# Kernel optimization log

Measured on AMD Instinct MI355X. Metric: run time of the kernel, lower is better.

## Reference

```python
import jax, jax.numpy as jnp
import numpy as np

T = 10            # inference steps (PCLayer.T)
LOCAL_LR = 0.001  # local_learning_rate
CLAMP = 1.0       # PCLayer.clamp_value


def setup_inputs() -> dict:
    key = jax.random.key(0)
    k1, k2 = jax.random.split(key)
    B, S, H_out, H_in = 8, 1024, 3072, 768
    target_activity = jax.random.normal(k1, (B, S, H_out), dtype=jnp.float32)
    # nn.Linear(H_in, H_out) weight: [H_out, H_in]
    W = jax.random.normal(k2, (H_out, H_in), dtype=jnp.float32) * (1.0 / np.sqrt(H_in))
    b = jnp.zeros((H_out,), dtype=jnp.float32)
    return {"target_activity": target_activity, "W": W, "b": b}


def reference(target_activity, W, b):
    # PCLayer forward, layer_type='fc1' (linear): T-step energy-gradient
    # fixed-point inference on latent x of shape [B, S, H_in].
    B, S, _ = target_activity.shape
    H_in = W.shape[1]
    x0 = jnp.zeros((B, S, H_in), dtype=target_activity.dtype)  # x_init

    def step(x, _):
        mu = jnp.einsum('bsi,oi->bso', x, W) + b       # prediction [B,S,H_out]
        err = target_activity - mu                      # prediction error
        # x <- x - lr * dE/dx, E = 0.5*||err||^2  =>  dE/dx = -err @ W
        x = x + LOCAL_LR * jnp.einsum('bso,oi->bsi', err, W)
        x = jnp.clip(x, -CLAMP, CLAMP)
        return x, None

    x, _ = jax.lax.scan(step, x0, None, length=T)
    return x
```

## Files before the change

kernel.cpp:

```cpp
#include <hip/hip_runtime.h>
#include <stdint.h>


typedef short bf16x8 __attribute__((ext_vector_type(8)));
typedef float f32x4  __attribute__((ext_vector_type(4)));
typedef unsigned short u16;
typedef unsigned int uint_as1 __attribute__((address_space(1)));
typedef unsigned int uint_as3 __attribute__((address_space(3)));

__device__ __forceinline__ float bf2f(u16 u) {
  union { unsigned int i; float f; } x; x.i = ((unsigned int)u) << 16; return x.f;
}
__device__ __forceinline__ u16 f2bf(float f) {
  union { float f; unsigned int i; } x; x.f = f;
  unsigned int r = x.i + 0x7fffu + ((x.i >> 16) & 1u);
  return (u16)(r >> 16);
}
__device__ __forceinline__ void gl2lds16(const void* g, void* l) {
  __builtin_amdgcn_global_load_lds((uint_as1*)(uintptr_t)g,
                                   (uint_as3*)(uintptr_t)l, 16, 0, 0);
}

template<int NK, int EPI>
__global__ __launch_bounds__(256, 2)
void gemm_lds(const u16* __restrict__ A, const u16* __restrict__ B,
              float* __restrict__ Cf, u16* __restrict__ Cb,
              const u16* __restrict__ Yb, const float* __restrict__ biasp,
              float* __restrict__ cvec, float alpha, float beta, int K, int ldc)
{
  __shared__ u16 As[64 * 32 * NK];
  __shared__ u16 Bs[128 * 32 * NK];
  const int tid = threadIdx.x, w = tid >> 6, lane = tid & 63;
  const int lm = lane & 15, quad = lane >> 4;
  const int wm = w & 1, wn = w >> 1;
  const int m0 = blockIdx.x * 64, n0 = blockIdx.y * 128;
  const int r = lane >> 2, q = lane & 3;
  const u16* Ag = A + (long)(m0 + w * 16 + r) * K + q * 8;
  const u16* Bg = B + (long)(n0 + w * 32 + r) * K + q * 8;
  u16* Asl = As + w * 16 * 32;
  u16* Bsl = Bs + w * 1024;

  f32x4 acc[2][4] = {};

  for (int kk = 0; kk < K; kk += 32 * NK) {
#pragma unroll
    for (int h = 0; h < NK; ++h) {
      gl2lds16(Ag + kk + h * 32, Asl + h * 2048);
      gl2lds16(Bg + kk + h * 32, Bsl + h * 4096);
      gl2lds16(Bg + 16 * (long)K + kk + h * 32, Bsl + h * 4096 + 512);
    }
    __syncthreads();
#pragma unroll
    for (int h = 0; h < NK; ++h) {
      bf16x8 af[2], bv[4];
#pragma unroll
      for (int i = 0; i < 2; ++i)
        af[i] = *(const bf16x8*)(As + h * 2048 +
                                 (wm * 32 + i * 16 + lm) * 32 + quad * 8);
#pragma unroll
      for (int j = 0; j < 4; ++j)
        bv[j] = *(const bf16x8*)(Bs + h * 4096 +
                                 (wn * 64 + j * 16 + lm) * 32 + quad * 8);
#pragma unroll
      for (int i = 0; i < 2; ++i)
#pragma unroll
        for (int j = 0; j < 4; ++j)
          acc[i][j] = __builtin_amdgcn_mfma_f32_16x16x32_bf16(af[i], bv[j],
                                                              acc[i][j], 0, 0, 0);
    }
    __syncthreads();
  }

  const int rbase = m0 + wm * 32 + quad * 4;
  const int cbase = n0 + wn * 64 + lm;
  float bvals[4] = {};
  bool haveb = false;
  if constexpr (EPI == 3) {
#pragma unroll
    for (int j = 0; j < 4; ++j) bvals[j] = biasp[cbase + j * 16];
    haveb = (bvals[0] != 0.f) | (bvals[1] != 0.f) |
            (bvals[2] != 0.f) | (bvals[3] != 0.f);
  }
  float rowsum[2][4] = {};
#pragma unroll
  for (int i = 0; i < 2; ++i)
#pragma unroll
    for (int j = 0; j < 4; ++j) {
      const int col = cbase + j * 16;
#pragma unroll
      for (int rr = 0; rr < 4; ++rr) {
        const long idx = (long)(rbase + i * 16 + rr) * ldc + col;
        const float v = alpha * acc[i][j][rr];
        if constexpr (EPI == 3) {
          const u16 qv = f2bf(v + beta * bf2f(Yb[idx]));
          Cb[idx] = qv;
          rowsum[i][rr] += bf2f(qv) * bvals[j];
        } else if constexpr (EPI == 4) {
          Cb[idx] = f2bf(v + beta * Cf[idx]);
        } else {
          Cf[idx] = v;
          Cb[idx] = f2bf(v);
        }
      }
    }
  if constexpr (EPI == 3) {
    if (__any(haveb)) {
#pragma unroll
      for (int i = 0; i < 2; ++i)
#pragma unroll
        for (int rr = 0; rr < 4; ++rr) {
          float s = rowsum[i][rr];
          s += __shfl_xor(s, 1); s += __shfl_xor(s, 2);
          s += __shfl_xor(s, 4); s += __shfl_xor(s, 8);
          if (lm == 0) atomicAdd(&cvec[rbase + i * 16 + rr], s);
        }
    }
  }
}

__global__ void conv_w(const float* __restrict__ W, u16* __restrict__ WTb,
                       u16* __restrict__ Wb, float* __restrict__ cvec)
{
  __shared__ u16 lds[64 * 72];
  const int bt = blockIdx.x, tid = threadIdx.x;
  if (bt == 0) { cvec[tid] = 0.f; cvec[tid + 256] = 0.f; cvec[tid + 512] = 0.f; }
  const int o0 = (bt / 12) * 64, i0 = (bt % 12) * 64;
  const int ol = tid >> 2, cg4 = tid & 3;
#pragma unroll
  for (int p = 0; p < 4; ++p) {
    const float4 v = *(const float4*)(W + (long)(o0 + ol) * 768 + i0 + (cg4 + p * 4) * 4);
    const int ib = (cg4 + p * 4) * 4;
    lds[(ib + 0) * 72 + ol] = f2bf(v.x);
    lds[(ib + 1) * 72 + ol] = f2bf(v.y);
    lds[(ib + 2) * 72 + ol] = f2bf(v.z);
    lds[(ib + 3) * 72 + ol] = f2bf(v.w);
    ushort4 wo;
    wo.x = f2bf(v.x); wo.y = f2bf(v.y); wo.z = f2bf(v.z); wo.w = f2bf(v.w);
    ((ushort4*)(Wb + (long)(o0 + ol) * 768 + i0))[cg4 + p * 4] = wo;
  }
  __syncthreads();
  const int cl = tid >> 2, og = tid & 3;
  const u16* src = lds + cl * 72 + og * 16;
  u16* dst = WTb + (long)(i0 + cl) * 3072 + o0 + og * 16;
  ((ushort4*)dst)[0] = ((const ushort4*)src)[0];
  ((ushort4*)dst)[1] = ((const ushort4*)src)[1];
  ((ushort4*)dst)[2] = ((const ushort4*)src)[2];
  ((ushort4*)dst)[3] = ((const ushort4*)src)[3];
}

__global__ __launch_bounds__(256, 2)
void gemm_big(const float* __restrict__ T, const u16* __restrict__ B,
              const float* __restrict__ cvec, float* __restrict__ out)
{
  __shared__ u16 As[2 * 64 * 32];
  __shared__ u16 Bs[2 * 256 * 32];
  const int tid = threadIdx.x, w = tid >> 6, lane = tid & 63;
  const int lm = lane & 15, quad = lane >> 4;
  const int m0 = blockIdx.x * 64, n0 = blockIdx.y * 256;
  const int r = lane >> 2, q = lane & 3;
  const int qs = q ^ ((r >> 2) & 3);
  const u16* Bg = B + (long)(n0 + w * 64 + r) * 3072 + qs * 8;
  u16* Bsl = Bs + w * 64 * 32;
  const int arow = tid >> 4, kq = tid & 15;
  const float* Ag = T + (long)(m0 + arow) * 3072 + kq * 4;
  const int h_a = kq >> 3;
  const int chunk_a = ((kq & 7) >> 1) ^ ((arow >> 2) & 3);
  const int ks_a = chunk_a * 8 + (kq & 1) * 4;
  const int swr = (lm >> 2) & 3;

  f32x4 acc[4][4] = {};

  for (int kk = 0; kk < 3072; kk += 64) {
#pragma unroll
    for (int h = 0; h < 2; ++h)
#pragma unroll
      for (int l = 0; l < 4; ++l)
        gl2lds16(Bg + (long)(l * 16) * 3072 + kk + h * 32,
                 Bsl + h * 8192 + l * 512);
#pragma unroll
    for (int p = 0; p < 4; ++p) {
      const float4 v = *(const float4*)(Ag + (long)(p * 16) * 3072 + kk);
      short4 o;
      o.x = (short)f2bf(v.x); o.y = (short)f2bf(v.y);
      o.z = (short)f2bf(v.z); o.w = (short)f2bf(v.w);
      *(short4*)(As + h_a * 2048 + (arow + p * 16) * 32 + ks_a) = o;
    }
    __syncthreads();
#pragma unroll
    for (int h = 0; h < 2; ++h) {
      bf16x8 af[4], bv[4];
#pragma unroll
      for (int i = 0; i < 4; ++i)
        af[i] = *(const bf16x8*)(As + h * 2048 + (i * 16 + lm) * 32 +
                                 ((quad ^ swr) * 8));
#pragma unroll
      for (int j = 0; j < 4; ++j)
        bv[j] = *(const bf16x8*)(Bs + h * 8192 + (w * 64 + j * 16 + lm) * 32 +
                                 ((quad ^ swr) * 8));
#pragma unroll
      for (int i = 0; i < 4; ++i)
#pragma unroll
        for (int j = 0; j < 4; ++j)
          acc[i][j] = __builtin_amdgcn_mfma_f32_16x16x32_bf16(af[i], bv[j],
                                                              acc[i][j], 0, 0, 0);
    }
    __syncthreads();
  }

  const int rbase = m0 + quad * 4;
  const int cbase = n0 + w * 64 + lm;
  float cj[4];
#pragma unroll
  for (int j = 0; j < 4; ++j) cj[j] = cvec[cbase + j * 16];
#pragma unroll
  for (int i = 0; i < 4; ++i)
#pragma unroll
    for (int j = 0; j < 4; ++j)
#pragma unroll
      for (int rr = 0; rr < 4; ++rr)
        out[(long)(rbase + i * 16 + rr) * 768 + cbase + j * 16] =
            acc[i][j][rr] - cj[j];
}

extern "C" void kernel_launch(void* const* d_in, const int* in_sizes, int n_in,
                              void* d_out, int out_size, void* d_ws, size_t ws_size,
                              hipStream_t stream)
{
  const float* t    = (const float*)d_in[0];
  const float* W    = (const float*)d_in[1];
  const float* bias = (const float*)d_in[2];
  float* out = (float*)d_out;

  char* p = (char*)d_ws;
  u16*   WTb  = (u16*)(p + 0);
  u16*   Wb   = (u16*)(p + 4718592);
  float* Ef   = (float*)(p + 9437184);
  u16*   Eb   = (u16*)(p + 11796480);
  u16*   Spb  = (u16*)(p + 12976128);
  u16*   WMTb = (u16*)(p + 14155776);
  float* cvec = (float*)(p + 18874368);

  const float lr = 0.001f;

  conv_w<<<576, 256, 0, stream>>>(W, WTb, Wb, cvec);
  gemm_lds<2, 5><<<dim3(12, 6), 256, 0, stream>>>(
      WTb, WTb, Ef, Eb, nullptr, nullptr, nullptr, lr, 0.f, 3072, 768);
  gemm_lds<2, 4><<<dim3(12, 6), 256, 0, stream>>>(
      Eb, Eb, Ef, Spb, nullptr, nullptr, nullptr, 120.f, -45.f, 768, 768);
  gemm_lds<2, 3><<<dim3(12, 24), 256, 0, stream>>>(
      Spb, Wb, nullptr, WMTb, WTb, bias, cvec, lr, 0.01f, 768, 3072);
  gemm_big<<<dim3(128, 3), 256, 0, stream>>>(t, WMTb, cvec, out);
}
```

Measured before the change: 290.5 us.

## Double-buffer B tiles and prefetch A in gemm_big, raise NK in gemm_lds

gemm_big now keeps two LDS buffers for the B tile. It issues the next tile's global-to-LDS loads and the next A float4 loads before the current MFMA work, so memory latency overlaps with compute and one barrier per iteration can be dropped. The XOR swizzle on LDS reads and writes is removed, which simplifies addressing but may bring back LDS bank conflicts. The gemm_lds launches also change the NK template parameter from 2 to 4. Doubling the B buffer raises LDS use, which could lower occupancy.

```diff
diff --git a/kernel.cpp b/kernel.cpp
--- a/kernel.cpp
+++ b/kernel.cpp
@@ -153,50 +153,62 @@
               const float* __restrict__ cvec, float* __restrict__ out)
 {
   __shared__ u16 As[2 * 64 * 32];
-  __shared__ u16 Bs[2 * 256 * 32];
+  __shared__ u16 Bs[2][2 * 256 * 32];
   const int tid = threadIdx.x, w = tid >> 6, lane = tid & 63;
   const int lm = lane & 15, quad = lane >> 4;
   const int m0 = blockIdx.x * 64, n0 = blockIdx.y * 256;
   const int r = lane >> 2, q = lane & 3;
-  const int qs = q ^ ((r >> 2) & 3);
-  const u16* Bg = B + (long)(n0 + w * 64 + r) * 3072 + qs * 8;
-  u16* Bsl = Bs + w * 64 * 32;
+  const u16* Bg = B + (long)(n0 + w * 64 + r) * 3072 + q * 8;
   const int arow = tid >> 4, kq = tid & 15;
   const float* Ag = T + (long)(m0 + arow) * 3072 + kq * 4;
-  const int h_a = kq >> 3;
-  const int chunk_a = ((kq & 7) >> 1) ^ ((arow >> 2) & 3);
-  const int ks_a = chunk_a * 8 + (kq & 1) * 4;
-  const int swr = (lm >> 2) & 3;
+  const int h_a = kq >> 3, ks_a = (kq & 7) * 4;
+  u16* As_dst = As + h_a * 2048 + arow * 32 + ks_a;
 
   f32x4 acc[4][4] = {};
-
+  float4 av[4];
+
+#pragma unroll
+  for (int p = 0; p < 4; ++p)
+    av[p] = *(const float4*)(Ag + (long)(p * 16) * 3072);
+#pragma unroll
+  for (int h = 0; h < 2; ++h)
+#pragma unroll
+    for (int l = 0; l < 4; ++l)
+      gl2lds16(Bg + (long)(l * 16) * 3072 + h * 32,
+               Bs[0] + h * 8192 + w * 2048 + l * 512);
+#pragma unroll
+  for (int p = 0; p < 4; ++p) {
+    short4 o;
+    o.x = (short)f2bf(av[p].x); o.y = (short)f2bf(av[p].y);
+    o.z = (short)f2bf(av[p].z); o.w = (short)f2bf(av[p].w);
+    *(short4*)(As_dst + p * 512) = o;
+  }
+
+  int buf = 0;
   for (int kk = 0; kk < 3072; kk += 64) {
-#pragma unroll
-    for (int h = 0; h < 2; ++h)
-#pragma unroll
-      for (int l = 0; l < 4; ++l)
-        gl2lds16(Bg + (long)(l * 16) * 3072 + kk + h * 32,
-                 Bsl + h * 8192 + l * 512);
-#pragma unroll
-    for (int p = 0; p < 4; ++p) {
-      const float4 v = *(const float4*)(Ag + (long)(p * 16) * 3072 + kk);
-      short4 o;
-      o.x = (short)f2bf(v.x); o.y = (short)f2bf(v.y);
-      o.z = (short)f2bf(v.z); o.w = (short)f2bf(v.w);
-      *(short4*)(As + h_a * 2048 + (arow + p * 16) * 32 + ks_a) = o;
-    }
     __syncthreads();
+    const bool haveNext = (kk + 64 < 3072);
+    if (haveNext) {
+#pragma unroll
+      for (int h = 0; h < 2; ++h)
+#pragma unroll
+        for (int l = 0; l < 4; ++l)
+          gl2lds16(Bg + (long)(l * 16) * 3072 + kk + 64 + h * 32,
+                   Bs[buf ^ 1] + h * 8192 + w * 2048 + l * 512);
+#pragma unroll
+      for (int p = 0; p < 4; ++p)
+        av[p] = *(const float4*)(Ag + (long)(p * 16) * 3072 + kk + 64);
+    }
+    const u16* Bsb = Bs[buf];
 #pragma unroll
     for (int h = 0; h < 2; ++h) {
       bf16x8 af[4], bv[4];
 #pragma unroll
       for (int i = 0; i < 4; ++i)
-        af[i] = *(const bf16x8*)(As + h * 2048 + (i * 16 + lm) * 32 +
-                                 ((quad ^ swr) * 8));
+        af[i] = *(const bf16x8*)(As + h * 2048 + (i * 16 + lm) * 32 + quad * 8);
 #pragma unroll
       for (int j = 0; j < 4; ++j)
-        bv[j] = *(const bf16x8*)(Bs + h * 8192 + (w * 64 + j * 16 + lm) * 32 +
-                                 ((quad ^ swr) * 8));
+        bv[j] = *(const bf16x8*)(Bsb + h * 8192 + (w * 64 + j * 16 + lm) * 32 + quad * 8);
 #pragma unroll
       for (int i = 0; i < 4; ++i)
 #pragma unroll
@@ -204,7 +216,17 @@
           acc[i][j] = __builtin_amdgcn_mfma_f32_16x16x32_bf16(af[i], bv[j],
                                                               acc[i][j], 0, 0, 0);
     }
-    __syncthreads();
+    if (haveNext) {
+      __syncthreads();
+#pragma unroll
+      for (int p = 0; p < 4; ++p) {
+        short4 o;
+        o.x = (short)f2bf(av[p].x); o.y = (short)f2bf(av[p].y);
+        o.z = (short)f2bf(av[p].z); o.w = (short)f2bf(av[p].w);
+        *(short4*)(As_dst + p * 512) = o;
+      }
+      buf ^= 1;
+    }
   }
 
   const int rbase = m0 + quad * 4;
@@ -243,11 +265,11 @@
   const float lr = 0.001f;
 
   conv_w<<<576, 256, 0, stream>>>(W, WTb, Wb, cvec);
-  gemm_lds<2, 5><<<dim3(12, 6), 256, 0, stream>>>(
+  gemm_lds<4, 5><<<dim3(12, 6), 256, 0, stream>>>(
       WTb, WTb, Ef, Eb, nullptr, nullptr, nullptr, lr, 0.f, 3072, 768);
-  gemm_lds<2, 4><<<dim3(12, 6), 256, 0, stream>>>(
+  gemm_lds<4, 4><<<dim3(12, 6), 256, 0, stream>>>(
       Eb, Eb, Ef, Spb, nullptr, nullptr, nullptr, 120.f, -45.f, 768, 768);
-  gemm_lds<2, 3><<<dim3(12, 24), 256, 0, stream>>>(
+  gemm_lds<4, 3><<<dim3(12, 24), 256, 0, stream>>>(
       Spb, Wb, nullptr, WMTb, WTb, bias, cvec, lr, 0.01f, 768, 3072);
   gemm_big<<<dim3(128, 3), 256, 0, stream>>>(t, WMTb, cvec, out);
 }
```

Result: faster. 281.4 us (-3.1%).

## Overlap target bf16 conversion with small GEMMs and reuse gemm_lds for final GEMM

Applied to the files above, without the earlier changes.

The fp32→bf16 conversion of the large target tensor, with bias subtracted, is split into slices run by extra blocks appended to the conv_w and three small GEMM launches. Those launches use only 72–288 blocks and leave most CUs idle, so the conversion uses that spare capacity. The final GEMM drops the specialized gemm_big, which converted fp32 inline, and becomes a gemm_lds instance with a new epilogue reading the pre-converted bf16 buffer. It also raises NK to 4 for all GEMMs. The cost is an extra 50MB bf16 buffer in workspace that is written and then read back.

```diff
diff --git a/kernel.cpp b/kernel.cpp
--- a/kernel.cpp
+++ b/kernel.cpp
@@ -21,19 +21,42 @@
                                    (uint_as3*)(uintptr_t)l, 16, 0, 0);
 }
 
+__device__ __forceinline__ void conv_slice(const float* __restrict__ t,
+                                           const float* __restrict__ bias,
+                                           u16* __restrict__ tb,
+                                           int blockUnit, int tid)
+{
+  const long i4 = (long)blockUnit * 256 + tid;
+  const float4 v = ((const float4*)t)[i4];
+  const float4 bb = ((const float4*)bias)[(int)(i4 % 768)];
+  ushort4 o;
+  o.x = f2bf(v.x - bb.x); o.y = f2bf(v.y - bb.y);
+  o.z = f2bf(v.z - bb.z); o.w = f2bf(v.w - bb.w);
+  ((ushort4*)tb)[i4] = o;
+}
+
 template<int NK, int EPI>
 __global__ __launch_bounds__(256, 2)
 void gemm_lds(const u16* __restrict__ A, const u16* __restrict__ B,
               float* __restrict__ Cf, u16* __restrict__ Cb,
               const u16* __restrict__ Yb, const float* __restrict__ biasp,
-              float* __restrict__ cvec, float alpha, float beta, int K, int ldc)
+              float* __restrict__ cvec, float alpha, float beta,
+              int K, int ldc, int nbx, int gemmBlocks, int convBase,
+              const float* __restrict__ tsrc, const float* __restrict__ tbias,
+              u16* __restrict__ tbdst)
 {
   __shared__ u16 As[64 * 32 * NK];
   __shared__ u16 Bs[128 * 32 * NK];
-  const int tid = threadIdx.x, w = tid >> 6, lane = tid & 63;
+  const int tid = threadIdx.x;
+  if ((int)blockIdx.x >= gemmBlocks) {
+    conv_slice(tsrc, tbias, tbdst, (int)blockIdx.x - gemmBlocks + convBase, tid);
+    return;
+  }
+  const int bx = (int)blockIdx.x % nbx, by = (int)blockIdx.x / nbx;
+  const int w = tid >> 6, lane = tid & 63;
   const int lm = lane & 15, quad = lane >> 4;
   const int wm = w & 1, wn = w >> 1;
-  const int m0 = blockIdx.x * 64, n0 = blockIdx.y * 128;
+  const int m0 = bx * 64, n0 = by * 128;
   const int r = lane >> 2, q = lane & 3;
   const u16* Ag = A + (long)(m0 + w * 16 + r) * K + q * 8;
   const u16* Bg = B + (long)(n0 + w * 32 + r) * K + q * 8;
@@ -80,6 +103,11 @@
     for (int j = 0; j < 4; ++j) bvals[j] = biasp[cbase + j * 16];
     haveb = (bvals[0] != 0.f) | (bvals[1] != 0.f) |
             (bvals[2] != 0.f) | (bvals[3] != 0.f);
+  }
+  float cj[4];
+  if constexpr (EPI == 6) {
+#pragma unroll
+    for (int j = 0; j < 4; ++j) cj[j] = cvec[cbase + j * 16];
   }
   float rowsum[2][4] = {};
 #pragma unroll
@@ -97,9 +125,11 @@
           rowsum[i][rr] += bf2f(qv) * bvals[j];
         } else if constexpr (EPI == 4) {
           Cb[idx] = f2bf(v + beta * Cf[idx]);
-        } else {
+        } else if constexpr (EPI == 5) {
           Cf[idx] = v;
           Cb[idx] = f2bf(v);
+        } else {
+          Cf[idx] = v - cj[j];
         }
       }
     }
@@ -118,11 +148,14 @@
   }
 }
 
-__global__ void conv_w(const float* __restrict__ W, u16* __restrict__ WTb,
-                       u16* __restrict__ Wb, float* __restrict__ cvec)
+__global__ void conv_w(const float* __restrict__ W, const float* __restrict__ t,
+                       const float* __restrict__ bias, u16* __restrict__ WTb,
+                       u16* __restrict__ Wb, u16* __restrict__ tb,
+                       float* __restrict__ cvec)
 {
   __shared__ u16 lds[64 * 72];
   const int bt = blockIdx.x, tid = threadIdx.x;
+  if (bt >= 576) { conv_slice(t, bias, tb, bt - 576, tid); return; }
   if (bt == 0) { cvec[tid] = 0.f; cvec[tid + 256] = 0.f; cvec[tid + 512] = 0.f; }
   const int o0 = (bt / 12) * 64, i0 = (bt % 12) * 64;
   const int ol = tid >> 2, cg4 = tid & 3;
@@ -148,80 +181,6 @@
   ((ushort4*)dst)[3] = ((const ushort4*)src)[3];
 }
 
-__global__ __launch_bounds__(256, 2)
-void gemm_big(const float* __restrict__ T, const u16* __restrict__ B,
-              const float* __restrict__ cvec, float* __restrict__ out)
-{
-  __shared__ u16 As[2 * 64 * 32];
-  __shared__ u16 Bs[2 * 256 * 32];
-  const int tid = threadIdx.x, w = tid >> 6, lane = tid & 63;
-  const int lm = lane & 15, quad = lane >> 4;
-  const int m0 = blockIdx.x * 64, n0 = blockIdx.y * 256;
-  const int r = lane >> 2, q = lane & 3;
-  const int qs = q ^ ((r >> 2) & 3);
-  const u16* Bg = B + (long)(n0 + w * 64 + r) * 3072 + qs * 8;
-  u16* Bsl = Bs + w * 64 * 32;
-  const int arow = tid >> 4, kq = tid & 15;
-  const float* Ag = T + (long)(m0 + arow) * 3072 + kq * 4;
-  const int h_a = kq >> 3;
-  const int chunk_a = ((kq & 7) >> 1) ^ ((arow >> 2) & 3);
-  const int ks_a = chunk_a * 8 + (kq & 1) * 4;
-  const int swr = (lm >> 2) & 3;
-
-  f32x4 acc[4][4] = {};
-
-  for (int kk = 0; kk < 3072; kk += 64) {
-#pragma unroll
-    for (int h = 0; h < 2; ++h)
-#pragma unroll
-      for (int l = 0; l < 4; ++l)
-        gl2lds16(Bg + (long)(l * 16) * 3072 + kk + h * 32,
-                 Bsl + h * 8192 + l * 512);
-#pragma unroll
-    for (int p = 0; p < 4; ++p) {
-      const float4 v = *(const float4*)(Ag + (long)(p * 16) * 3072 + kk);
-      short4 o;
-      o.x = (short)f2bf(v.x); o.y = (short)f2bf(v.y);
-      o.z = (short)f2bf(v.z); o.w = (short)f2bf(v.w);
-      *(short4*)(As + h_a * 2048 + (arow + p * 16) * 32 + ks_a) = o;
-    }
-    __syncthreads();
-#pragma unroll
-    for (int h = 0; h < 2; ++h) {
-      bf16x8 af[4], bv[4];
-#pragma unroll
-      for (int i = 0; i < 4; ++i)
-        af[i] = *(const bf16x8*)(As + h * 2048 + (i * 16 + lm) * 32 +
-                                 ((quad ^ swr) * 8));
-#pragma unroll
-      for (int j = 0; j < 4; ++j)
-        bv[j] = *(const bf16x8*)(Bs + h * 8192 + (w * 64 + j * 16 + lm) * 32 +
-                                 ((quad ^ swr) * 8));
-#pragma unroll
-      for (int i = 0; i < 4; ++i)
-#pragma unroll
-        for (int j = 0; j < 4; ++j)
-          acc[i][j] = __builtin_amdgcn_mfma_f32_16x16x32_bf16(af[i], bv[j],
-                                                              acc[i][j], 0, 0, 0);
-    }
-    __syncthreads();
-  }
-
-  const int rbase = m0 + quad * 4;
-  const int cbase = n0 + w * 64 + lm;
-  float cj[4];
-#pragma unroll
-  for (int j = 0; j < 4; ++j) cj[j] = cvec[cbase + j * 16];
-#pragma unroll
-  for (int i = 0; i < 4; ++i)
-#pragma unroll
-    for (int j = 0; j < 4; ++j)
-#pragma unroll
-      for (int rr = 0; rr < 4; ++rr)
-        out[(long)(rbase + i * 16 + rr) * 768 + cbase + j * 16] =
-            acc[i][j][rr] - cj[j];
-}
-
 extern "C" void kernel_launch(void* const* d_in, const int* in_sizes, int n_in,
                               void* d_out, int out_size, void* d_ws, size_t ws_size,
                               hipStream_t stream)
@@ -232,22 +191,28 @@
   float* out = (float*)d_out;
 
   char* p = (char*)d_ws;
-  u16*   WTb  = (u16*)(p + 0);
-  u16*   Wb   = (u16*)(p + 4718592);
-  float* Ef   = (float*)(p + 9437184);
-  u16*   Eb   = (u16*)(p + 11796480);
-  u16*   Spb  = (u16*)(p + 12976128);
-  u16*   WMTb = (u16*)(p + 14155776);
-  float* cvec = (float*)(p + 18874368);
+  u16*   tb   = (u16*)(p + 0);
+  u16*   WTb  = (u16*)(p + 50331648);
+  u16*   Wb   = (u16*)(p + 55050240);
+  float* Ef   = (float*)(p + 59768832);
+  u16*   Eb   = (u16*)(p + 62128128);
+  u16*   Spb  = (u16*)(p + 63307776);
+  u16*   WMTb = (u16*)(p + 64487424);
+  float* cvec = (float*)(p + 69206016);
 
   const float lr = 0.001f;
 
-  conv_w<<<576, 256, 0, stream>>>(W, WTb, Wb, cvec);
-  gemm_lds<2, 5><<<dim3(12, 6), 256, 0, stream>>>(
-      WTb, WTb, Ef, Eb, nullptr, nullptr, nullptr, lr, 0.f, 3072, 768);
-  gemm_lds<2, 4><<<dim3(12, 6), 256, 0, stream>>>(
-      Eb, Eb, Ef, Spb, nullptr, nullptr, nullptr, 120.f, -45.f, 768, 768);
-  gemm_lds<2, 3><<<dim3(12, 24), 256, 0, stream>>>(
-      Spb, Wb, nullptr, WMTb, WTb, bias, cvec, lr, 0.01f, 768, 3072);
-  gemm_big<<<dim3(128, 3), 256, 0, stream>>>(t, WMTb, cvec, out);
-}
+  conv_w<<<576 + 6144, 256, 0, stream>>>(W, t, bias, WTb, Wb, tb, cvec);
+  gemm_lds<4, 5><<<72 + 6144, 256, 0, stream>>>(
+      WTb, WTb, Ef, Eb, nullptr, nullptr, nullptr, lr, 0.f, 3072, 768,
+      12, 72, 6144, t, bias, tb);
+  gemm_lds<4, 4><<<72 + 6144, 256, 0, stream>>>(
+      Eb, Eb, Ef, Spb, nullptr, nullptr, nullptr, 120.f, -45.f, 768, 768,
+      12, 72, 12288, t, bias, tb);
+  gemm_lds<4, 3><<<288 + 6144, 256, 0, stream>>>(
+      Spb, Wb, nullptr, WMTb, WTb, bias, cvec, lr, 0.01f, 768, 3072,
+      12, 288, 18432, t, bias, tb);
+  gemm_lds<4, 6><<<768, 256, 0, stream>>>(
+      tb, WMTb, out, nullptr, nullptr, nullptr, cvec, 1.f, 0.f, 3072, 768,
+      128, 768, 0, nullptr, nullptr, nullptr);
+}
```

Result: faster. 274.3 us (-5.6%).
